# Optimization experiments

Hardware: AMD Instinct MI355X
Metric: run time of the kernel (lower is better)

## Reference

```python
import jax, jax.numpy as jnp
import numpy as np

N, E, H = 50000, 800000, 128
EIN = 2 * H + 1  # edge MLP input: h[row] | h[col] | radial_norm


def _mk(key, shape, scale=0.02):
    return jax.random.normal(key, shape, dtype=jnp.float32) * scale


def setup_inputs() -> dict:
    key = jax.random.key(0)
    ks = jax.random.split(key, 20)
    h = jax.random.normal(ks[0], (N, H), dtype=jnp.float32)
    pos = jax.random.normal(ks[1], (N, 3), dtype=jnp.float32)
    edge_index = jax.random.randint(ks[2], (2, E), 0, N, dtype=jnp.int64)
    return {
        "h": h, "pos": pos, "edge_index": edge_index,
        # edge_mlp: Linear(EIN,H) -> SiLU -> Linear(H,H)
        "We1": _mk(ks[3], (H, EIN)), "be1": jnp.zeros((H,), jnp.float32),
        "We2": _mk(ks[4], (H, H)),   "be2": jnp.zeros((H,), jnp.float32),
        # node_mlp: Linear(2H,H) -> SiLU -> Linear(H,H)
        "Wn1": _mk(ks[5], (H, 2 * H)), "bn1": jnp.zeros((H,), jnp.float32),
        "Wn2": _mk(ks[6], (H, H)),     "bn2": jnp.zeros((H,), jnp.float32),
        # coord_mlp: Linear(H,H) -> SiLU -> Linear(H,1)
        "Wc1": _mk(ks[7], (H, H)), "bc1": jnp.zeros((H,), jnp.float32),
        "Wc2": _mk(ks[8], (1, H)), "bc2": jnp.zeros((1,), jnp.float32),
    }


def reference(h, pos, edge_index, We1, be1, We2, be2, Wn1, bn1, Wn2, bn2, Wc1, bc1, Wc2, bc2):
    row, col = edge_index[0], edge_index[1]
    radial = pos[row] - pos[col]                                   # [E,3]
    radial_norm = jnp.maximum(
        jnp.linalg.norm(radial, axis=-1, keepdims=True), 1e-8)     # [E,1]
    edge_input = jnp.concatenate([h[row], h[col], radial_norm], -1)  # [E,2H+1]
    m_ij = jax.nn.silu(edge_input @ We1.T + be1) @ We2.T + be2      # [E,H]
    agg = jax.ops.segment_sum(m_ij, row, num_segments=h.shape[0])   # [N,H]
    node_in = jnp.concatenate([h, agg], -1)                         # [N,2H]
    h_new = h + (jax.nn.silu(node_in @ Wn1.T + bn1) @ Wn2.T + bn2)
    coord_diff = jnp.tanh(jax.nn.silu(m_ij @ Wc1.T + bc1) @ Wc2.T + bc2) * 0.1  # [E,1]
    coord_update = coord_diff * (radial / radial_norm)              # [E,3]
    pos_new = pos.at[row].add(coord_update)
    return h_new, pos_new
```

## Files before the change

### kernel.cpp

```cpp
#include <hip/hip_runtime.h>
#include <math.h>

#define N_NODES 50000
#define N_EDGES 800000
#define H 128
#define EIN 257
#define EPB 64
#define NWG_EDGE (N_EDGES / EPB)
#define CNT_PAD 50176
#define NBS 196

typedef short bf16x8 __attribute__((ext_vector_type(8)));
typedef short bf16x4 __attribute__((ext_vector_type(4)));
typedef short bf16x2 __attribute__((ext_vector_type(2)));
typedef float f32x4 __attribute__((ext_vector_type(4)));

static __device__ __forceinline__ short f2bf(float x) {
    unsigned u = __builtin_bit_cast(unsigned, x);
    unsigned r = (u + 0x7FFFu + ((u >> 16) & 1u)) >> 16;
    return (short)r;
}

static __device__ __forceinline__ short f2bfr(float x) {
    return (short)((__builtin_bit_cast(unsigned, x) + 0x8000u) >> 16);
}

static __device__ __forceinline__ float bf2f(short s) {
    return __builtin_bit_cast(float, ((unsigned)(unsigned short)s) << 16);
}

static __device__ __forceinline__ float silu(float x) {
#if __has_builtin(__builtin_amdgcn_rcpf)
    return x * __builtin_amdgcn_rcpf(1.0f + __expf(-x));
#else
    return x / (1.0f + __expf(-x));
#endif
}

static __device__ __forceinline__ void pk_agg_add(unsigned* addr, unsigned val) {
#if __has_builtin(__builtin_amdgcn_global_atomic_fadd_v2bf16)
    bf16x2 v = __builtin_bit_cast(bf16x2, val);
    (void)__builtin_amdgcn_global_atomic_fadd_v2bf16(
        (__attribute__((address_space(1))) bf16x2*)(unsigned long long)addr, v);
#else
    asm volatile("global_atomic_pk_add_bf16 %0, %1, off"
                 :: "v"(addr), "v"(val) : "memory");
#endif
}

#define P_W1  (128*264)
#define P_W2  (128*128)
#define P_TOT (2*(P_W1 + P_W2))
#define NH4   (N_NODES * H / 4)
#define AGG16 (N_NODES * H * 2 / 16)
#define POS4  ((N_NODES * 3 + 3) / 4)
#define NW3   (128*128)
#define PROJ_NB ((N_NODES + 63) / 64)

__global__ __launch_bounds__(256) void prep_w(
    const float* __restrict__ We1, const float* __restrict__ We2,
    const float* __restrict__ Wc1, const float* __restrict__ be2,
    const float* __restrict__ bc1,
    const float* __restrict__ Wn1, const float* __restrict__ Wn2,
    short* __restrict__ W1b, short* __restrict__ W2b, short* __restrict__ W3b,
    short* __restrict__ Wn1b, short* __restrict__ Wn2b,
    float* __restrict__ w256f, float* __restrict__ bc1p,
    unsigned* __restrict__ cnt, int cntn)
{
    int i = blockIdx.x * 256 + threadIdx.x;
    if (i < P_TOT) {
        if (i < P_W1) {
            int j = i / 264, k = i % 264;
            W1b[i] = (k < EIN) ? f2bf(We1[j * EIN + k]) : (short)0;
        } else if (i < P_W1 + P_W2) {
            int t = i - P_W1;
            W2b[t] = f2bf(We2[t]);
        } else if (i < 2 * P_W1 + P_W2) {
            int t = i - P_W1 - P_W2;
            int j = t / 264, k = t % 264;
            Wn1b[t] = (k < 256) ? f2bf(Wn1[j * 256 + k]) : (short)0;
        } else {
            int t = i - 2 * P_W1 - P_W2;
            Wn2b[t] = f2bf(Wn2[t]);
        }
        return;
    }
    i -= P_TOT;
    if (i < 128) { w256f[i] = We1[i * EIN + 256]; return; }
    i -= 128;
    if (i < NW3) {
        int j = i >> 7, k = i & 127;
        const float* wr = &Wc1[j * 128];
        float acc = 0.f;
        #pragma unroll 8
        for (int o = 0; o < 128; ++o)
            acc += wr[o] * We2[o * 128 + k];
        W3b[i] = f2bf(acc);
        return;
    }
    i -= NW3;
    if (i < 128) {
        const float* wr = &Wc1[i * 128];
        float acc = bc1[i];
        #pragma unroll 8
        for (int o = 0; o < 128; ++o) acc += wr[o] * be2[o];
        bc1p[i] = acc;
        return;
    }
    i -= 128;
    if (cnt && i < cntn) cnt[i] = 0u;
}

template<bool PROJ_ON>
__global__ __launch_bounds__(256) void prep2(
    int proj_nb,
    const float* __restrict__ h, const short* __restrict__ W1b,
    const float* __restrict__ be1,
    short* __restrict__ Abf, short* __restrict__ Bbf,
    int nh4, short* __restrict__ hbf,
    uint4* __restrict__ aggz, int aggz_n,
    float4* __restrict__ pos_dst, const float4* __restrict__ pos_src,
    const int* __restrict__ erow, unsigned* __restrict__ cnt)
{
    const int tid = threadIdx.x;
    if (PROJ_ON && (int)blockIdx.x < proj_nb) {
        __shared__ short hh[64][136];
        const int nb = blockIdx.x * 64;
        {
            const int rlane = tid & 15;
            const int row0  = tid >> 4;
            #pragma unroll
            for (int it = 0; it < 4; ++it) {
                int rr = row0 + it * 16;
                int node = nb + rr;
                if (node >= N_NODES) node = N_NODES - 1;
                const float4* src = (const float4*)&h[(size_t)node * H + rlane * 8];
                float4 a = src[0], b = src[1];
                bf16x8 v = { f2bf(a.x), f2bf(a.y), f2bf(a.z), f2bf(a.w),
                             f2bf(b.x), f2bf(b.y), f2bf(b.z), f2bf(b.w) };
                *(bf16x8*)&hh[rr][rlane * 8] = v;
            }
        }
        __syncthreads();

        const int lane = tid & 63;
        const int q    = lane >> 4;
        const int l15  = lane & 15;
        const int n0   = (tid >> 6) * 32;

        f32x4 accA[2][4] = {}, accB[2][4] = {};
        #pragma unroll
        for (int ks = 0; ks < 4; ++ks) {
            int k0 = ks * 32 + q * 8;
            bf16x8 wa0 = *(const bf16x8*)&W1b[(n0 + l15) * 264 + k0];
            bf16x8 wa1 = *(const bf16x8*)&W1b[(n0 + 16 + l15) * 264 + k0];
            bf16x8 wb0 = *(const bf16x8*)&W1b[(n0 + l15) * 264 + 128 + k0];
            bf16x8 wb1 = *(const bf16x8*)&W1b[(n0 + 16 + l15) * 264 + 128 + k0];
            bf16x8 e0 = *(const bf16x8*)&hh[l15][k0];
            bf16x8 e1 = *(const bf16x8*)&hh[16 + l15][k0];
// ... 64 lines not shown
    unsigned v = (i < N_NODES) ? cnt[i] : 0u;
    unsigned orig = v;
    #pragma unroll
    for (int d = 1; d < 64; d <<= 1) {
        unsigned n = __shfl_up(v, d);
        if ((t & 63) >= d) v += n;
    }
    __shared__ unsigned wsum[4], woff[4];
    if ((t & 63) == 63) wsum[t >> 6] = v;
    __syncthreads();
    if (t == 0) {
        unsigned r = 0;
        #pragma unroll
        for (int k = 0; k < 4; ++k) { woff[k] = r; r += wsum[k]; }
    }
    __syncthreads();
    unsigned incl = v + woff[t >> 6];
    offs[i] = incl - orig;
    if (t == 255) bsum[blockIdx.x] = incl;
}

__global__ __launch_bounds__(256) void scatter_edges(const int* __restrict__ eidx,
        unsigned* __restrict__ offs, const unsigned* __restrict__ bsum,
        int2* __restrict__ es) {
    __shared__ unsigned sb[256];
    __shared__ unsigned wsum[4], woff[4];
    int t = threadIdx.x;
    unsigned v = (t < NBS) ? bsum[t] : 0u;
    unsigned orig = v;
    #pragma unroll
    for (int d = 1; d < 64; d <<= 1) {
        unsigned n = __shfl_up(v, d);
        if ((t & 63) >= d) v += n;
    }
    if ((t & 63) == 63) wsum[t >> 6] = v;
    __syncthreads();
    if (t == 0) {
        unsigned r = 0;
        #pragma unroll
        for (int k = 0; k < 4; ++k) { woff[k] = r; r += wsum[k]; }
    }
    __syncthreads();
    sb[t] = v + woff[t >> 6] - orig;
    __syncthreads();
    int e = blockIdx.x * 256 + t;
    if (e < N_EDGES) {
        int r = eidx[e];
        unsigned p = atomicAdd(&offs[r], 1u) + sb[r >> 8];
        es[p] = int2{r, eidx[N_EDGES + e]};
    }
}

template<bool AGGBF16, bool SORTED, bool PROJ>
__global__ __launch_bounds__(256, 4) void edge_kernel(
    const short* __restrict__ hbf,
    const short* __restrict__ Abf, const short* __restrict__ Bbf,
    const float* __restrict__ pos,
    const int2* __restrict__ es,
    const int* __restrict__ rsrc, const int* __restrict__ csrc,
    const float* __restrict__ w256f, const float* __restrict__ be1,
    const float* __restrict__ be2, const float* __restrict__ bc1p,
    const float* __restrict__ wc2f, const float* __restrict__ bc2,
    const short* __restrict__ W1b, const short* __restrict__ W2b,
    const short* __restrict__ W3b,
    unsigned* __restrict__ aggb,
    float* __restrict__ aggf,
    float* __restrict__ pos_out)
{
    __shared__ union {
        short ein[EPB][264];
        struct { short t[EPB][136]; short m[EPB][136]; } p;
    } s_u;
    __shared__ float s_rn[EPB];
    __shared__ float s_unit[EPB][3];
    __shared__ int   s_row[EPB];
    __shared__ int   s_col[EPB];
    __shared__ float s_dot[EPB];

    const int tid = threadIdx.x;

    int wg;
    {
        const int Q = NWG_EDGE >> 3, R = NWG_EDGE & 7;
        int x = blockIdx.x & 7, k = blockIdx.x >> 3;
        int start = (x < R) ? x * (Q + 1) : R * (Q + 1) + (x - R) * Q;
        wg = start + k;
    }
    const int eb = wg * EPB;

    if (tid < EPB) {
        int ge = eb + tid;
        int r, c;
        if constexpr (SORTED) { int2 rc = es[ge]; r = rc.x; c = rc.y; }
        else { r = rsrc[ge]; c = csrc[ge]; }
        s_row[tid] = r;
        s_col[tid] = c;
        float dx = pos[r*3+0] - pos[c*3+0];
        float dy = pos[r*3+1] - pos[c*3+1];
        float dz = pos[r*3+2] - pos[c*3+2];
        float nrm = sqrtf(dx*dx + dy*dy + dz*dz);
        float rn  = fmaxf(nrm, 1e-8f);
        s_rn[tid] = rn;
        s_unit[tid][0] = dx / rn;
        s_unit[tid][1] = dy / rn;
        s_unit[tid][2] = dz / rn;
        s_dot[tid] = 0.0f;
    }
    __syncthreads();

    const int lane = tid & 63;
    const int q    = lane >> 4;
    const int l15  = lane & 15;
    const int n0   = (tid >> 6) * 32;
    const int w    = tid >> 6;
    const int rlane = tid & 15;
    const int row0  = tid >> 4;

    if constexpr (PROJ) {
        float4 wv0 = *(const float4*)&w256f[rlane * 8];
        float4 wv1 = *(const float4*)&w256f[rlane * 8 + 4];
        float wv[8] = { wv0.x, wv0.y, wv0.z, wv0.w, wv1.x, wv1.y, wv1.z, wv1.w };
        #pragma unroll
        for (int it = 0; it < 4; ++it) {
            int e = row0 + it * 16;
            bf16x8 a = *(const bf16x8*)&Abf[(size_t)s_row[e] * H + rlane * 8];
            bf16x8 b = *(const bf16x8*)&Bbf[(size_t)s_col[e] * H + rlane * 8];
            float rn = s_rn[e];
            bf16x8 t8;
            #pragma unroll
            for (int j = 0; j < 8; ++j) {
                float x = bf2f(a[j]) + bf2f(b[j]) + rn * wv[j];
                t8[j] = f2bfr(silu(x));
            }
            *(bf16x8*)&s_u.p.t[e][rlane * 8] = t8;
        }
    } else {
        #pragma unroll
        for (int it = 0; it < 8; ++it) {
            int rr = row0 + it * 16;
            int e  = rr & 63, sg = rr >> 6;
            int idx = sg ? s_col[e] : s_row[e];
            bf16x8 v = *(const bf16x8*)&hbf[(size_t)idx * H + rlane * 8];
            *(bf16x8*)&s_u.ein[e][sg * 128 + rlane * 8] = v;
        }
        __syncthreads();

        f32x4 acc[2][4] = {};
        #pragma unroll
        for (int ks = 0; ks < 8; ++ks) {
            int k0 = ks * 32 + q * 8;
            bf16x8 w0 = *(const bf16x8*)&W1b[(n0 + l15) * 264 + k0];
            bf16x8 w1 = *(const bf16x8*)&W1b[(n0 + 16 + l15) * 264 + k0];
            bf16x8 e0 = *(const bf16x8*)&s_u.ein[l15][k0];
            bf16x8 e1 = *(const bf16x8*)&s_u.ein[16 + l15][k0];
            bf16x8 e2 = *(const bf16x8*)&s_u.ein[32 + l15][k0];
            bf16x8 e3 = *(const bf16x8*)&s_u.ein[48 + l15][k0];
            acc[0][0] = __builtin_amdgcn_mfma_f32_16x16x32_bf16(w0, e0, acc[0][0], 0, 0, 0);
            acc[0][1] = __builtin_amdgcn_mfma_f32_16x16x32_bf16(w0, e1, acc[0][1], 0, 0, 0);
            acc[0][2] = __builtin_amdgcn_mfma_f32_16x16x32_bf16(w0, e2, acc[0][2], 0, 0, 0);
            acc[0][3] = __builtin_amdgcn_mfma_f32_16x16x32_bf16(w0, e3, acc[0][3], 0, 0, 0);
            acc[1][0] = __builtin_amdgcn_mfma_f32_16x16x32_bf16(w1, e0, acc[1][0], 0, 0, 0);
            acc[1][1] = __builtin_amdgcn_mfma_f32_16x16x32_bf16(w1, e1, acc[1][1], 0, 0, 0);
            acc[1][2] = __builtin_amdgcn_mfma_f32_16x16x32_bf16(w1, e2, acc[1][2], 0, 0, 0);
            acc[1][3] = __builtin_amdgcn_mfma_f32_16x16x32_bf16(w1, e3, acc[1][3], 0, 0, 0);
        }
        float w256v[2][4], b1v[2][4], rn_e[4];
        #pragma unroll
        for (int ct = 0; ct < 2; ++ct)
            #pragma unroll
            for (int r = 0; r < 4; ++r) {
                int ch = n0 + ct * 16 + q * 4 + r;
                w256v[ct][r] = w256f[ch];
                b1v[ct][r]   = be1[ch];
            }
        #pragma unroll
        for (int et = 0; et < 4; ++et) rn_e[et] = s_rn[et * 16 + l15];

        bf16x4 tv[2][4];
        #pragma unroll
        for (int ct = 0; ct < 2; ++ct)
            #pragma unroll
            for (int et = 0; et < 4; ++et) {
                bf16x4 v;
                #pragma unroll
                for (int r = 0; r < 4; ++r)
                    v[r] = f2bfr(silu(acc[ct][et][r] + rn_e[et] * w256v[ct][r] + b1v[ct][r]));
                tv[ct][et] = v;
            }
        __syncthreads();
        #pragma unroll
        for (int ct = 0; ct < 2; ++ct)
            #pragma unroll
            for (int et = 0; et < 4; ++et)
                *(bf16x4*)&s_u.p.t[et * 16 + l15][n0 + ct * 16 + q * 4] = tv[ct][et];
    }
    __syncthreads();

    f32x4 acc2[2][4] = {}, acc3[2][4] = {};
    #pragma unroll
    for (int ks = 0; ks < 4; ++ks) {
        int k0 = ks * 32 + q * 8;
        bf16x8 w20 = *(const bf16x8*)&W2b[(n0 + l15) * 128 + k0];
        bf16x8 w21 = *(const bf16x8*)&W2b[(n0 + 16 + l15) * 128 + k0];
        bf16x8 w30 = *(const bf16x8*)&W3b[(n0 + l15) * 128 + k0];
        bf16x8 w31 = *(const bf16x8*)&W3b[(n0 + 16 + l15) * 128 + k0];
        bf16x8 e0 = *(const bf16x8*)&s_u.p.t[l15][k0];
        bf16x8 e1 = *(const bf16x8*)&s_u.p.t[16 + l15][k0];
        bf16x8 e2 = *(const bf16x8*)&s_u.p.t[32 + l15][k0];
        bf16x8 e3 = *(const bf16x8*)&s_u.p.t[48 + l15][k0];
        acc2[0][0] = __builtin_amdgcn_mfma_f32_16x16x32_bf16(w20, e0, acc2[0][0], 0, 0, 0);
        acc2[0][1] = __builtin_amdgcn_mfma_f32_16x16x32_bf16(w20, e1, acc2[0][1], 0, 0, 0);
        acc2[0][2] = __builtin_amdgcn_mfma_f32_16x16x32_bf16(w20, e2, acc2[0][2], 0, 0, 0);
        acc2[0][3] = __builtin_amdgcn_mfma_f32_16x16x32_bf16(w20, e3, acc2[0][3], 0, 0, 0);
        acc2[1][0] = __builtin_amdgcn_mfma_f32_16x16x32_bf16(w21, e0, acc2[1][0], 0, 0, 0);
        acc2[1][1] = __builtin_amdgcn_mfma_f32_16x16x32_bf16(w21, e1, acc2[1][1], 0, 0, 0);
        acc2[1][2] = __builtin_amdgcn_mfma_f32_16x16x32_bf16(w21, e2, acc2[1][2], 0, 0, 0);
        acc2[1][3] = __builtin_amdgcn_mfma_f32_16x16x32_bf16(w21, e3, acc2[1][3], 0, 0, 0);
        acc3[0][0] = __builtin_amdgcn_mfma_f32_16x16x32_bf16(w30, e0, acc3[0][0], 0, 0, 0);
        acc3[0][1] = __builtin_amdgcn_mfma_f32_16x16x32_bf16(w30, e1, acc3[0][1], 0, 0, 0);
        acc3[0][2] = __builtin_amdgcn_mfma_f32_16x16x32_bf16(w30, e2, acc3[0][2], 0, 0, 0);
        acc3[0][3] = __builtin_amdgcn_mfma_f32_16x16x32_bf16(w30, e3, acc3[0][3], 0, 0, 0);
        acc3[1][0] = __builtin_amdgcn_mfma_f32_16x16x32_bf16(w31, e0, acc3[1][0], 0, 0, 0);
        acc3[1][1] = __builtin_amdgcn_mfma_f32_16x16x32_bf16(w31, e1, acc3[1][1], 0, 0, 0);
        acc3[1][2] = __builtin_amdgcn_mfma_f32_16x16x32_bf16(w31, e2, acc3[1][2], 0, 0, 0);
        acc3[1][3] = __builtin_amdgcn_mfma_f32_16x16x32_bf16(w31, e3, acc3[1][3], 0, 0, 0);
    }

    {
        float b2v[2][4];
        #pragma unroll
        for (int ct = 0; ct < 2; ++ct)
            #pragma unroll
            for (int r = 0; r < 4; ++r)
                b2v[ct][r] = be2[n0 + ct * 16 + q * 4 + r];
        #pragma unroll
        for (int ct = 0; ct < 2; ++ct)
            #pragma unroll
            for (int et = 0; et < 4; ++et) {
                bf16x4 v;
                #pragma unroll
                for (int r = 0; r < 4; ++r)
                    v[r] = f2bfr(acc2[ct][et][r] + b2v[ct][r]);
                *(bf16x4*)&s_u.p.m[et * 16 + l15][n0 + ct * 16 + q * 4] = v;
            }
    }

    {
        float p[4] = {0.f, 0.f, 0.f, 0.f};
        #pragma unroll
        for (int ct = 0; ct < 2; ++ct)
            #pragma unroll
            for (int r = 0; r < 4; ++r) {
                int ch = n0 + ct * 16 + q * 4 + r;
                float bias = bc1p[ch];
                float w2   = wc2f[ch];
                #pragma unroll
                for (int et = 0; et < 4; ++et)
                    p[et] += silu(acc3[ct][et][r] + bias) * w2;
            }
        #pragma unroll
        for (int et = 0; et < 4; ++et) {
            float v = p[et];
            v += __shfl_xor(v, 16);
            v += __shfl_xor(v, 32);
            if (q == et) atomicAdd(&s_dot[et * 16 + l15], v);
        }
    }
    __syncthreads();

    if constexpr (AGGBF16) {
        const int base = w * 16;
        float a0 = 0.f, a1 = 0.f;
        int cur = s_row[base];
        #pragma unroll
        for (int i = 0; i < 16; ++i) {
            int nd = s_row[base + i];
            if (nd != cur) {
                unsigned pk = ((unsigned)(unsigned short)f2bfr(a0)) |
                              (((unsigned)(unsigned short)f2bfr(a1)) << 16);
                pk_agg_add(&aggb[(size_t)cur * 64 + lane], pk);
                a0 = 0.f; a1 = 0.f; cur = nd;
            }
            unsigned pr = *(const unsigned*)&s_u.p.m[base + i][lane * 2];
            a0 += __builtin_bit_cast(float, pr << 16);
            a1 += __builtin_bit_cast(float, pr & 0xFFFF0000u);
        }
        unsigned pk = ((unsigned)(unsigned short)f2bfr(a0)) |
                      (((unsigned)(unsigned short)f2bfr(a1)) << 16);
        pk_agg_add(&aggb[(size_t)cur * 64 + lane], pk);
    } else {
        #pragma unroll
        for (int i = 0; i < 16; ++i) {
            int row = w + i * 4;
            unsigned pr = *(const unsigned*)&s_u.p.m[row][lane * 2];
            float f0 = __builtin_bit_cast(float, pr << 16);
            float f1 = __builtin_bit_cast(float, pr & 0xFFFF0000u);
            float* dst = &aggf[(size_t)s_row[row] * H + 2 * lane];
            atomicAdd(dst, f0);
            atomicAdd(dst + 1, f1);
        }
    }

    if (tid < EPB) {
        float s = tanhf(s_dot[tid] + bc2[0]) * 0.1f;
        s_unit[tid][0] *= s;
        s_unit[tid][1] *= s;
        s_unit[tid][2] *= s;
    }
    __syncthreads();
    if (tid < EPB) {
        int r = s_row[tid];
        bool last = (tid == EPB - 1) || (s_row[tid + 1] != r);
        if (last) {
            float sx = 0.f, sy = 0.f, sz = 0.f;
            for (int j = tid; j >= 0 && s_row[j] == r; --j) {
                sx += s_unit[j][0];
                sy += s_unit[j][1];
                sz += s_unit[j][2];
            }
            atomicAdd(&pos_out[r * 3 + 0], sx);
            atomicAdd(&pos_out[r * 3 + 1], sy);
            atomicAdd(&pos_out[r * 3 + 2], sz);
        }
    }
}

template<bool AGGBF16>
__global__ __launch_bounds__(256) void node_kernel(
    const float* __restrict__ h,
    const unsigned short* __restrict__ aggb, const float* __restrict__ aggf,
    const float* __restrict__ bn1, const float* __restrict__ bn2,
    const short* __restrict__ Wn1b, const short* __restrict__ Wn2b,
    float* __restrict__ hout)
{
    __shared__ short s_a[64][264];
    __shared__ short s_t[64][136];

    const int tid = threadIdx.x;
    const int nb  = blockIdx.x * 64;

    {
        const int rlane = tid & 15;
        const int row0  = tid >> 4;
        #pragma unroll
        for (int it = 0; it < 8; ++it) {
            int rr = row0 + it * 16;
            int e  = rr & 63, sg = rr >> 6;
            int node = nb + e;
            if (node >= N_NODES) node = N_NODES - 1;
            bf16x8 v;
            if (sg == 0) {
                const float4* src = (const float4*)&h[(size_t)node * H + rlane * 8];
                float4 a = src[0], b = src[1];
                v = bf16x8{ f2bf(a.x), f2bf(a.y), f2bf(a.z), f2bf(a.w),
                            f2bf(b.x), f2bf(b.y), f2bf(b.z), f2bf(b.w) };
            } else if constexpr (AGGBF16) {
                v = *(const bf16x8*)&aggb[(size_t)node * H + rlane * 8];
            } else {
                const float* src = &aggf[(size_t)node * H + rlane * 8];
                bf16x8 t;
                #pragma unroll
                for (int j = 0; j < 8; ++j) t[j] = f2bfr(src[j]);
                v = t;
            }
            *(bf16x8*)&s_a[e][sg * 128 + rlane * 8] = v;
        }
    }
    __syncthreads();

    const int lane = tid & 63;
    const int q    = lane >> 4;
    const int l15  = lane & 15;
    const int n0   = (tid >> 6) * 32;

    f32x4 acc[2][4] = {};
    #pragma unroll
    for (int ks = 0; ks < 8; ++ks) {
        int k0 = ks * 32 + q * 8;
        bf16x8 w0 = *(const bf16x8*)&Wn1b[(n0 + l15) * 264 + k0];
        bf16x8 w1 = *(const bf16x8*)&Wn1b[(n0 + 16 + l15) * 264 + k0];
        bf16x8 e0 = *(const bf16x8*)&s_a[l15][k0];
        bf16x8 e1 = *(const bf16x8*)&s_a[16 + l15][k0];
        bf16x8 e2 = *(const bf16x8*)&s_a[32 + l15][k0];
        bf16x8 e3 = *(const bf16x8*)&s_a[48 + l15][k0];
        acc[0][0] = __builtin_amdgcn_mfma_f32_16x16x32_bf16(w0, e0, acc[0][0], 0, 0, 0);
        acc[0][1] = __builtin_amdgcn_mfma_f32_16x16x32_bf16(w0, e1, acc[0][1], 0, 0, 0);
        acc[0][2] = __builtin_amdgcn_mfma_f32_16x16x32_bf16(w0, e2, acc[0][2], 0, 0, 0);
        acc[0][3] = __builtin_amdgcn_mfma_f32_16x16x32_bf16(w0, e3, acc[0][3], 0, 0, 0);
        acc[1][0] = __builtin_amdgcn_mfma_f32_16x16x32_bf16(w1, e0, acc[1][0], 0, 0, 0);
        acc[1][1] = __builtin_amdgcn_mfma_f32_16x16x32_bf16(w1, e1, acc[1][1], 0, 0, 0);
        acc[1][2] = __builtin_amdgcn_mfma_f32_16x16x32_bf16(w1, e2, acc[1][2], 0, 0, 0);
        acc[1][3] = __builtin_amdgcn_mfma_f32_16x16x32_bf16(w1, e3, acc[1][3], 0, 0, 0);
    }
    {
        float b1v[2][4];
        #pragma unroll
        for (int ct = 0; ct < 2; ++ct)
            #pragma unroll
            for (int r = 0; r < 4; ++r)
                b1v[ct][r] = bn1[n0 + ct * 16 + q * 4 + r];
        #pragma unroll
        for (int ct = 0; ct < 2; ++ct)
            #pragma unroll
            for (int et = 0; et < 4; ++et) {
                bf16x4 v;
                #pragma unroll
                for (int r = 0; r < 4; ++r)
                    v[r] = f2bfr(silu(acc[ct][et][r] + b1v[ct][r]));
                *(bf16x4*)&s_t[et * 16 + l15][n0 + ct * 16 + q * 4] = v;
            }
    }
    __syncthreads();

    f32x4 acc2[2][4] = {};
    #pragma unroll
    for (int ks = 0; ks < 4; ++ks) {
        int k0 = ks * 32 + q * 8;
        bf16x8 w0 = *(const bf16x8*)&Wn2b[(n0 + l15) * 128 + k0];
        bf16x8 w1 = *(const bf16x8*)&Wn2b[(n0 + 16 + l15) * 128 + k0];
        bf16x8 e0 = *(const bf16x8*)&s_t[l15][k0];
        bf16x8 e1 = *(const bf16x8*)&s_t[16 + l15][k0];
        bf16x8 e2 = *(const bf16x8*)&s_t[32 + l15][k0];
        bf16x8 e3 = *(const bf16x8*)&s_t[48 + l15][k0];
        acc2[0][0] = __builtin_amdgcn_mfma_f32_16x16x32_bf16(w0, e0, acc2[0][0], 0, 0, 0);
        acc2[0][1] = __builtin_amdgcn_mfma_f32_16x16x32_bf16(w0, e1, acc2[0][1], 0, 0, 0);
        acc2[0][2] = __builtin_amdgcn_mfma_f32_16x16x32_bf16(w0, e2, acc2[0][2], 0, 0, 0);
        acc2[0][3] = __builtin_amdgcn_mfma_f32_16x16x32_bf16(w0, e3, acc2[0][3], 0, 0, 0);
        acc2[1][0] = __builtin_amdgcn_mfma_f32_16x16x32_bf16(w1, e0, acc2[1][0], 0, 0, 0);
        acc2[1][1] = __builtin_amdgcn_mfma_f32_16x16x32_bf16(w1, e1, acc2[1][1], 0, 0, 0);
        acc2[1][2] = __builtin_amdgcn_mfma_f32_16x16x32_bf16(w1, e2, acc2[1][2], 0, 0, 0);
        acc2[1][3] = __builtin_amdgcn_mfma_f32_16x16x32_bf16(w1, e3, acc2[1][3], 0, 0, 0);
    }
    {
        float b2v[2][4];
        #pragma unroll
        for (int ct = 0; ct < 2; ++ct)
            #pragma unroll
            for (int r = 0; r < 4; ++r)
                b2v[ct][r] = bn2[n0 + ct * 16 + q * 4 + r];
        #pragma unroll
        for (int ct = 0; ct < 2; ++ct)
            #pragma unroll
            for (int et = 0; et < 4; ++et) {
                int node = nb + et * 16 + l15;
                if (node < N_NODES) {
                    int ch0 = n0 + ct * 16 + q * 4;
                    const float4 hres = *(const float4*)&h[(size_t)node * H + ch0];
                    float4 o;
                    o.x = acc2[ct][et][0] + b2v[ct][0] + hres.x;
                    o.y = acc2[ct][et][1] + b2v[ct][1] + hres.y;
                    o.z = acc2[ct][et][2] + b2v[ct][2] + hres.z;
                    o.w = acc2[ct][et][3] + b2v[ct][3] + hres.w;
                    *(float4*)&hout[(size_t)node * H + ch0] = o;
                }
            }
    }
}

extern "C" void kernel_launch(void* const* d_in, const int* in_sizes, int n_in,
                              void* d_out, int out_size, void* d_ws, size_t ws_size,
                              hipStream_t stream) {
    const float* h   = (const float*)d_in[0];
    const float* pos = (const float*)d_in[1];
    const int*  eidx = (const int*)d_in[2];
    const float* We1 = (const float*)d_in[3];
    const float* be1 = (const float*)d_in[4];
    const float* We2 = (const float*)d_in[5];
    const float* be2 = (const float*)d_in[6];
    const float* Wn1 = (const float*)d_in[7];
    const float* bn1 = (const float*)d_in[8];
    const float* Wn2 = (const float*)d_in[9];
    const float* bn2 = (const float*)d_in[10];
    const float* Wc1 = (const float*)d_in[11];
    const float* bc1 = (const float*)d_in[12];
    const float* Wc2 = (const float*)d_in[13];
    const float* bc2 = (const float*)d_in[14];

    float* out_h   = (float*)d_out;
    float* out_pos = out_h + (size_t)N_NODES * H;

    char* ws = (char*)d_ws;
    short* W1b  = (short*)(ws);
    short* W2b  = (short*)(ws + 2 * P_W1);
    short* W3b  = (short*)(ws + 2 * (P_W1 + P_W2));
    short* Wn1b = (short*)(ws + 2 * (P_W1 + 2 * P_W2));
    short* Wn2b = (short*)(ws + 2 * (2 * P_W1 + 2 * P_W2));
    float* w256f = (float*)(ws + 2 * (size_t)(2 * P_W1 + 3 * P_W2));
    float* bc1p  = w256f + 128;
    const size_t WSW = 2 * (size_t)(2 * P_W1 + 3 * P_W2) + 1024;
    const size_t HBF = (size_t)N_NODES * H * 2;
    const size_t AGG = (size_t)N_NODES * H * 2;
    const size_t CNTB = (size_t)CNT_PAD * 4;
    const size_t BSB  = 256 * 4;
    const size_t ESB  = (size_t)N_EDGES * 8;
    const size_t PRJ  = (size_t)N_NODES * H * 2;
    short* hbf = (short*)(ws + WSW);
    const bool use_bf16 = (ws_size >= WSW + HBF + AGG);
    const bool use_sort = (ws_size >= WSW + HBF + AGG + CNTB + BSB + ESB);
    const bool use_proj = (ws_size >= WSW + HBF + AGG + CNTB + BSB + ESB + 2 * PRJ);

    const int PW_N  = P_TOT + 128 + NW3 + 128;

    if (use_bf16) {
        unsigned* aggb = (unsigned*)(ws + WSW + HBF);
        if (use_sort) {
            unsigned* cnt  = (unsigned*)(ws + WSW + HBF + AGG);
            unsigned* bsum = (unsigned*)((char*)cnt + CNTB);
            int2* es = (int2*)((char*)bsum + BSB);
            short* Abf = (short*)((char*)es + ESB);
            short* Bbf = (short*)((char*)Abf + PRJ);

            prep_w<<<(PW_N + CNT_PAD + 255) / 256, 256, 0, stream>>>(
                We1, We2, Wc1, be2, bc1, Wn1, Wn2,
                W1b, W2b, W3b, Wn1b, Wn2b, w256f, bc1p, cnt, CNT_PAD);
            if (use_proj) {
                const int rest = AGG16 + POS4 + N_EDGES;
                prep2<true><<<PROJ_NB + (rest + 255) / 256, 256, 0, stream>>>(
                    PROJ_NB, h, W1b, be1, Abf, Bbf, 0, nullptr,
                    (uint4*)aggb, AGG16, (float4*)out_pos, (const float4*)pos,
                    eidx, cnt);
            } else {
                const int rest = NH4 + AGG16 + POS4 + N_EDGES;
                prep2<false><<<(rest + 255) / 256, 256, 0, stream>>>(
                    0, h, nullptr, nullptr, nullptr, nullptr, NH4, hbf,
                    (uint4*)aggb, AGG16, (float4*)out_pos, (const float4*)pos,
                    eidx, cnt);
            }
            scan1<<<NBS, 256, 0, stream>>>(cnt, cnt, bsum);
            scatter_edges<<<(N_EDGES + 255) / 256, 256, 0, stream>>>(eidx, cnt, bsum, es);
            if (use_proj)
                edge_kernel<true, true, true><<<NWG_EDGE, 256, 0, stream>>>(
                    hbf, Abf, Bbf, pos, es, nullptr, nullptr,
                    w256f, be1, be2, bc1p, Wc2, bc2,
                    W1b, W2b, W3b, aggb, nullptr, out_pos);
            else
                edge_kernel<true, true, false><<<NWG_EDGE, 256, 0, stream>>>(
                    hbf, nullptr, nullptr, pos, es, nullptr, nullptr,
                    w256f, be1, be2, bc1p, Wc2, bc2,
                    W1b, W2b, W3b, aggb, nullptr, out_pos);
        } else {
            prep_w<<<(PW_N + 255) / 256, 256, 0, stream>>>(
                We1, We2, Wc1, be2, bc1, Wn1, Wn2,
                W1b, W2b, W3b, Wn1b, Wn2b, w256f, bc1p, nullptr, 0);
            const int rest = NH4 + AGG16 + POS4;
            prep2<false><<<(rest + 255) / 256, 256, 0, stream>>>(
                0, h, nullptr, nullptr, nullptr, nullptr, NH4, hbf,
                (uint4*)aggb, AGG16, (float4*)out_pos, (const float4*)pos,
                nullptr, nullptr);
            edge_kernel<true, false, false><<<NWG_EDGE, 256, 0, stream>>>(
                hbf, nullptr, nullptr, pos, nullptr, eidx, eidx + N_EDGES,
                w256f, be1, be2, bc1p, Wc2, bc2,
                W1b, W2b, W3b, aggb, nullptr, out_pos);
        }
        node_kernel<true><<<(N_NODES + 63) / 64, 256, 0, stream>>>(
            h, (const unsigned short*)aggb, nullptr,
            bn1, bn2, Wn1b, Wn2b, out_h);
    } else {
        prep_w<<<(PW_N + 255) / 256, 256, 0, stream>>>(
            We1, We2, Wc1, be2, bc1, Wn1, Wn2,
            W1b, W2b, W3b, Wn1b, Wn2b, w256f, bc1p, nullptr, 0);
        const int rest = NH4 + POS4;
        prep2<false><<<(rest + 255) / 256, 256, 0, stream>>>(
            0, h, nullptr, nullptr, nullptr, nullptr, NH4, hbf,
            nullptr, 0, (float4*)out_pos, (const float4*)pos,
            nullptr, nullptr);
        hipMemsetAsync(out_h, 0, (size_t)N_NODES * H * sizeof(float), stream);
        edge_kernel<false, false, false><<<NWG_EDGE, 256, 0, stream>>>(
            hbf, nullptr, nullptr, pos, nullptr, eidx, eidx + N_EDGES,
            w256f, be1, be2, bc1p, Wc2, bc2,
            W1b, W2b, W3b, nullptr, out_h, out_pos);
        node_kernel<false><<<(N_NODES + 63) / 64, 256, 0, stream>>>(
            h, nullptr, out_h, bn1, bn2, Wn1b, Wn2b, out_h);
    }
}
```

Baseline: 412.7 us.

## Fold second edge-MLP layer into node MLP, aggregate pre-activation edge hidden state

Linearity lets segment_sum be pushed through We2: the edge kernel now scatters the silu hidden state t instead of m_ij. The node kernel uses Wn1·We2 as a folded weight and adds degree × (Wn1·be2) as a bias. This removes the per-edge W2 GEMM and the m staging in LDS on the projection path, keeping only the coord GEMM. A separate offsets buffer keeps the raw degree counts, and launch bounds rise to 8 waves per SIMD because LDS use drops. The fold adds bf16 rounding in a different place, and the higher occupancy target may force register spills.

New measurement: 354.3 us. 14.1% less time.

```diff
diff --git a/kernel.cpp b/kernel.cpp
--- a/kernel.cpp
+++ b/kernel.cpp
@@ -65,7 +65,8 @@
     short* __restrict__ W1b, short* __restrict__ W2b, short* __restrict__ W3b,
     short* __restrict__ Wn1b, short* __restrict__ Wn2b,
     float* __restrict__ w256f, float* __restrict__ bc1p,
-    unsigned* __restrict__ cnt, int cntn)
+    float* __restrict__ bfold,
+    unsigned* __restrict__ cnt, int cntn, int fold)
 {
     int i = blockIdx.x * 256 + threadIdx.x;
     if (i < P_TOT) {
@@ -78,7 +79,19 @@
         } else if (i < 2 * P_W1 + P_W2) {
             int t = i - P_W1 - P_W2;
             int j = t / 264, k = t % 264;
-            Wn1b[t] = (k < 256) ? f2bf(Wn1[j * 256 + k]) : (short)0;
+            short v;
+            if (k < 128) v = f2bf(Wn1[j * 256 + k]);
+            else if (k < 256) {
+                if (fold) {
+                    const float* wr = &Wn1[j * 256 + 128];
+                    const float* wc = &We2[k - 128];
+                    float acc = 0.f;
+                    #pragma unroll 8
+                    for (int o = 0; o < 128; ++o) acc += wr[o] * wc[o * 128];
+                    v = f2bf(acc);
+                } else v = f2bf(Wn1[j * 256 + k]);
+            } else v = 0;
+            Wn1b[t] = v;
         } else {
             int t = i - 2 * P_W1 - P_W2;
             Wn2b[t] = f2bf(Wn2[t]);
@@ -105,6 +118,15 @@
         #pragma unroll 8
         for (int o = 0; o < 128; ++o) acc += wr[o] * be2[o];
         bc1p[i] = acc;
+        return;
+    }
+    i -= 128;
+    if (i < 128) {
+        const float* wr = &Wn1[i * 256 + 128];
+        float acc = 0.f;
+        #pragma unroll 8
+        for (int o = 0; o < 128; ++o) acc += wr[o] * be2[o];
+        bfold[i] = acc;
         return;
     }
     i -= 128;
@@ -275,7 +297,7 @@
 }
 
 template<bool AGGBF16, bool SORTED, bool PROJ>
-__global__ __launch_bounds__(256, 4) void edge_kernel(
+__global__ __launch_bounds__(256, 8) void edge_kernel(
     const short* __restrict__ hbf,
     const short* __restrict__ Abf, const short* __restrict__ Bbf,
     const float* __restrict__ pos,
@@ -290,10 +312,7 @@
     float* __restrict__ aggf,
     float* __restrict__ pos_out)
 {
-    __shared__ union {
-        short ein[EPB][264];
-        struct { short t[EPB][136]; short m[EPB][136]; } p;
-    } s_u;
+    __shared__ short s_t[EPB][136];
     __shared__ float s_rn[EPB];
     __shared__ float s_unit[EPB][3];
     __shared__ int   s_row[EPB];
@@ -355,16 +374,83 @@
                 float x = bf2f(a[j]) + bf2f(b[j]) + rn * wv[j];
                 t8[j] = f2bfr(silu(x));
             }
-            *(bf16x8*)&s_u.p.t[e][rlane * 8] = t8;
-        }
+            *(bf16x8*)&s_t[e][rlane * 8] = t8;
+        }
+        __syncthreads();
+
+        {
+            const int base = w * 16;
+            float a0 = 0.f, a1 = 0.f;
+            int cur = s_row[base];
+            #pragma unroll
+            for (int i = 0; i < 16; ++i) {
+                int nd = s_row[base + i];
+                if (nd != cur) {
+                    unsigned pk = ((unsigned)(unsigned short)f2bfr(a0)) |
+                                  (((unsigned)(unsigned short)f2bfr(a1)) << 16);
+                    pk_agg_add(&aggb[(size_t)cur * 64 + lane], pk);
+                    a0 = 0.f; a1 = 0.f; cur = nd;
+                }
+                unsigned pr = *(const unsigned*)&s_t[base + i][lane * 2];
+                a0 += __builtin_bit_cast(float, pr << 16);
+                a1 += __builtin_bit_cast(float, pr & 0xFFFF0000u);
+            }
+            unsigned pk = ((unsigned)(unsigned short)f2bfr(a0)) |
+                          (((unsigned)(unsigned short)f2bfr(a1)) << 16);
+            pk_agg_add(&aggb[(size_t)cur * 64 + lane], pk);
+        }
+
+        f32x4 acc3[2][4] = {};
+        #pragma unroll
+        for (int ks = 0; ks < 4; ++ks) {
+            int k0 = ks * 32 + q * 8;
+            bf16x8 w30 = *(const bf16x8*)&W3b[(n0 + l15) * 128 + k0];
+            bf16x8 w31 = *(const bf16x8*)&W3b[(n0 + 16 + l15) * 128 + k0];
+            bf16x8 e0 = *(const bf16x8*)&s_t[l15][k0];
+            bf16x8 e1 = *(const bf16x8*)&s_t[16 + l15][k0];
+            bf16x8 e2 = *(const bf16x8*)&s_t[32 + l15][k0];
+            bf16x8 e3 = *(const bf16x8*)&s_t[48 + l15][k0];
+            acc3[0][0] = __builtin_amdgcn_mfma_f32_16x16x32_bf16(w30, e0, acc3[0][0], 0, 0, 0);
+            acc3[0][1] = __builtin_amdgcn_mfma_f32_16x16x32_bf16(w30, e1, acc3[0][1], 0, 0, 0);
+            acc3[0][2] = __builtin_amdgcn_mfma_f32_16x16x32_bf16(w30, e2, acc3[0][2], 0, 0, 0);
+            acc3[0][3] = __builtin_amdgcn_mfma_f32_16x16x32_bf16(w30, e3, acc3[0][3], 0, 0, 0);
+            acc3[1][0] = __builtin_amdgcn_mfma_f32_16x16x32_bf16(w31, e0, acc3[1][0], 0, 0, 0);
+            acc3[1][1] = __builtin_amdgcn_mfma_f32_16x16x32_bf16(w31, e1, acc3[1][1], 0, 0, 0);
+            acc3[1][2] = __builtin_amdgcn_mfma_f32_16x16x32_bf16(w31, e2, acc3[1][2], 0, 0, 0);
+            acc3[1][3] = __builtin_amdgcn_mfma_f32_16x16x32_bf16(w31, e3, acc3[1][3], 0, 0, 0);
+        }
+        {
+            float p[4] = {0.f, 0.f, 0.f, 0.f};
+            #pragma unroll
+            for (int ct = 0; ct < 2; ++ct)
+                #pragma unroll
+                for (int r = 0; r < 4; ++r) {
+                    int ch = n0 + ct * 16 + q * 4 + r;
+                    float bias = bc1p[ch];
+                    float w2   = wc2f[ch];
+                    #pragma unroll
+                    for (int et = 0; et < 4; ++et)
+                        p[et] += silu(acc3[ct][et][r] + bias) * w2;
+                }
+            #pragma unroll
+            for (int et = 0; et < 4; ++et) {
+                float v = p[et];
+                v += __shfl_xor(v, 16);
+                v += __shfl_xor(v, 32);
+                if (q == et) atomicAdd(&s_dot[et * 16 + l15], v);
+            }
+        }
+        __syncthreads();
     } else {
+        __shared__ short s_ein[EPB][264];
+        __shared__ short s_m[EPB][136];
         #pragma unroll
         for (int it = 0; it < 8; ++it) {
             int rr = row0 + it * 16;
             int e  = rr & 63, sg = rr >> 6;
             int idx = sg ? s_col[e] : s_row[e];
             bf16x8 v = *(const bf16x8*)&hbf[(size_t)idx * H + rlane * 8];
-            *(bf16x8*)&s_u.ein[e][sg * 128 + rlane * 8] = v;
+            *(bf16x8*)&s_ein[e][sg * 128 + rlane * 8] = v;
         }
         __syncthreads();
 
@@ -374,10 +460,10 @@
             int k0 = ks * 32 + q * 8;
             bf16x8 w0 = *(const bf16x8*)&W1b[(n0 + l15) * 264 + k0];
             bf16x8 w1 = *(const bf16x8*)&W1b[(n0 + 16 + l15) * 264 + k0];
-            bf16x8 e0 = *(const bf16x8*)&s_u.ein[l15][k0];
-            bf16x8 e1 = *(const bf16x8*)&s_u.ein[16 + l15][k0];
-            bf16x8 e2 = *(const bf16x8*)&s_u.ein[32 + l15][k0];
-            bf16x8 e3 = *(const bf16x8*)&s_u.ein[48 + l15][k0];
+            bf16x8 e0 = *(const bf16x8*)&s_ein[l15][k0];
+            bf16x8 e1 = *(const bf16x8*)&s_ein[16 + l15][k0];
+            bf16x8 e2 = *(const bf16x8*)&s_ein[32 + l15][k0];
+            bf16x8 e3 = *(const bf16x8*)&s_ein[48 + l15][k0];
             acc[0][0] = __builtin_amdgcn_mfma_f32_16x16x32_bf16(w0, e0, acc[0][0], 0, 0, 0);
             acc[0][1] = __builtin_amdgcn_mfma_f32_16x16x32_bf16(w0, e1, acc[0][1], 0, 0, 0);
             acc[0][2] = __builtin_amdgcn_mfma_f32_16x16x32_bf16(w0, e2, acc[0][2], 0, 0, 0);
@@ -387,140 +473,132 @@
             acc[1][2] = __builtin_amdgcn_mfma_f32_16x16x32_bf16(w1, e2, acc[1][2], 0, 0, 0);
             acc[1][3] = __builtin_amdgcn_mfma_f32_16x16x32_bf16(w1, e3, acc[1][3], 0, 0, 0);
         }
-        float w256v[2][4], b1v[2][4], rn_e[4];
-        #pragma unroll
-        for (int ct = 0; ct < 2; ++ct)
-            #pragma unroll
-            for (int r = 0; r < 4; ++r) {
-                int ch = n0 + ct * 16 + q * 4 + r;
-                w256v[ct][r] = w256f[ch];
-                b1v[ct][r]   = be1[ch];
-            }
-        #pragma unroll
-        for (int et = 0; et < 4; ++et) rn_e[et] = s_rn[et * 16 + l15];
-
-        bf16x4 tv[2][4];
-        #pragma unroll
-        for (int ct = 0; ct < 2; ++ct)
-            #pragma unroll
-            for (int et = 0; et < 4; ++et) {
-                bf16x4 v;
+        {
+            float w256v[2][4], b1v[2][4], rn_e[4];
+            #pragma unroll
+            for (int ct = 0; ct < 2; ++ct)
+                #pragma unroll
+                for (int r = 0; r < 4; ++r) {
+                    int ch = n0 + ct * 16 + q * 4 + r;
+                    w256v[ct][r] = w256f[ch];
+                    b1v[ct][r]   = be1[ch];
+                }
+            #pragma unroll
+            for (int et = 0; et < 4; ++et) rn_e[et] = s_rn[et * 16 + l15];
+            #pragma unroll
+            for (int ct = 0; ct < 2; ++ct)
+                #pragma unroll
+                for (int et = 0; et < 4; ++et) {
+                    bf16x4 v;
+                    #pragma unroll
+                    for (int r = 0; r < 4; ++r)
+                        v[r] = f2bfr(silu(acc[ct][et][r] + rn_e[et] * w256v[ct][r] + b1v[ct][r]));
+                    *(bf16x4*)&s_t[et * 16 + l15][n0 + ct * 16 + q * 4] = v;
+                }
+        }
+        __syncthreads();
+
+        f32x4 acc2[2][4] = {}, acc3[2][4] = {};
+        #pragma unroll
+        for (int ks = 0; ks < 4; ++ks) {
+            int k0 = ks * 32 + q * 8;
+            bf16x8 w20 = *(const bf16x8*)&W2b[(n0 + l15) * 128 + k0];
+            bf16x8 w21 = *(const bf16x8*)&W2b[(n0 + 16 + l15) * 128 + k0];
+            bf16x8 w30 = *(const bf16x8*)&W3b[(n0 + l15) * 128 + k0];
+            bf16x8 w31 = *(const bf16x8*)&W3b[(n0 + 16 + l15) * 128 + k0];
+            bf16x8 e0 = *(const bf16x8*)&s_t[l15][k0];
+            bf16x8 e1 = *(const bf16x8*)&s_t[16 + l15][k0];
+            bf16x8 e2 = *(const bf16x8*)&s_t[32 + l15][k0];
+            bf16x8 e3 = *(const bf16x8*)&s_t[48 + l15][k0];
+            acc2[0][0] = __builtin_amdgcn_mfma_f32_16x16x32_bf16(w20, e0, acc2[0][0], 0, 0, 0);
+            acc2[0][1] = __builtin_amdgcn_mfma_f32_16x16x32_bf16(w20, e1, acc2[0][1], 0, 0, 0);
+            acc2[0][2] = __builtin_amdgcn_mfma_f32_16x16x32_bf16(w20, e2, acc2[0][2], 0, 0, 0);
+            acc2[0][3] = __builtin_amdgcn_mfma_f32_16x16x32_bf16(w20, e3, acc2[0][3], 0, 0, 0);
+            acc2[1][0] = __builtin_amdgcn_mfma_f32_16x16x32_bf16(w21, e0, acc2[1][0], 0, 0, 0);
+            acc2[1][1] = __builtin_amdgcn_mfma_f32_16x16x32_bf16(w21, e1, acc2[1][1], 0, 0, 0);
+            acc2[1][2] = __builtin_amdgcn_mfma_f32_16x16x32_bf16(w21, e2, acc2[1][2], 0, 0, 0);
+            acc2[1][3] = __builtin_amdgcn_mfma_f32_16x16x32_bf16(w21, e3, acc2[1][3], 0, 0, 0);
+            acc3[0][0] = __builtin_amdgcn_mfma_f32_16x16x32_bf16(w30, e0, acc3[0][0], 0, 0, 0);
+            acc3[0][1] = __builtin_amdgcn_mfma_f32_16x16x32_bf16(w30, e1, acc3[0][1], 0, 0, 0);
+            acc3[0][2] = __builtin_amdgcn_mfma_f32_16x16x32_bf16(w30, e2, acc3[0][2], 0, 0, 0);
+            acc3[0][3] = __builtin_amdgcn_mfma_f32_16x16x32_bf16(w30, e3, acc3[0][3], 0, 0, 0);
+            acc3[1][0] = __builtin_amdgcn_mfma_f32_16x16x32_bf16(w31, e0, acc3[1][0], 0, 0, 0);
+            acc3[1][1] = __builtin_amdgcn_mfma_f32_16x16x32_bf16(w31, e1, acc3[1][1], 0, 0, 0);
+            acc3[1][2] = __builtin_amdgcn_mfma_f32_16x16x32_bf16(w31, e2, acc3[1][2], 0, 0, 0);
+            acc3[1][3] = __builtin_amdgcn_mfma_f32_16x16x32_bf16(w31, e3, acc3[1][3], 0, 0, 0);
+        }
+        {
+            float b2v[2][4];
+            #pragma unroll
+            for (int ct = 0; ct < 2; ++ct)
                 #pragma unroll
                 for (int r = 0; r < 4; ++r)
-                    v[r] = f2bfr(silu(acc[ct][et][r] + rn_e[et] * w256v[ct][r] + b1v[ct][r]));
-                tv[ct][et] = v;
-            }
+                    b2v[ct][r] = be2[n0 + ct * 16 + q * 4 + r];
+            #pragma unroll
+            for (int ct = 0; ct < 2; ++ct)
+                #pragma unroll
+                for (int et = 0; et < 4; ++et) {
+                    bf16x4 v;
+                    #pragma unroll
+                    for (int r = 0; r < 4; ++r)
+                        v[r] = f2bfr(acc2[ct][et][r] + b2v[ct][r]);
+                    *(bf16x4*)&s_m[et * 16 + l15][n0 + ct * 16 + q * 4] = v;
+                }
+        }
+        {
+            float p[4] = {0.f, 0.f, 0.f, 0.f};
+            #pragma unroll
+            for (int ct = 0; ct < 2; ++ct)
+                #pragma unroll
+                for (int r = 0; r < 4; ++r) {
+                    int ch = n0 + ct * 16 + q * 4 + r;
+                    float bias = bc1p[ch];
+                    float w2   = wc2f[ch];
+                    #pragma unroll
+                    for (int et = 0; et < 4; ++et)
+                        p[et] += silu(acc3[ct][et][r] + bias) * w2;
+                }
+            #pragma unroll
+            for (int et = 0; et < 4; ++et) {
+                float v = p[et];
+                v += __shfl_xor(v, 16);
+                v += __shfl_xor(v, 32);
+                if (q == et) atomicAdd(&s_dot[et * 16 + l15], v);
+            }
+        }
         __syncthreads();
-        #pragma unroll
-        for (int ct = 0; ct < 2; ++ct)
-            #pragma unroll
-            for (int et = 0; et < 4; ++et)
-                *(bf16x4*)&s_u.p.t[et * 16 + l15][n0 + ct * 16 + q * 4] = tv[ct][et];
-    }
-    __syncthreads();
-
-    f32x4 acc2[2][4] = {}, acc3[2][4] = {};
-    #pragma unroll
-    for (int ks = 0; ks < 4; ++ks) {
-        int k0 = ks * 32 + q * 8;
-        bf16x8 w20 = *(const bf16x8*)&W2b[(n0 + l15) * 128 + k0];
-        bf16x8 w21 = *(const bf16x8*)&W2b[(n0 + 16 + l15) * 128 + k0];
-        bf16x8 w30 = *(const bf16x8*)&W3b[(n0 + l15) * 128 + k0];
-        bf16x8 w31 = *(const bf16x8*)&W3b[(n0 + 16 + l15) * 128 + k0];
-        bf16x8 e0 = *(const bf16x8*)&s_u.p.t[l15][k0];
-        bf16x8 e1 = *(const bf16x8*)&s_u.p.t[16 + l15][k0];
-        bf16x8 e2 = *(const bf16x8*)&s_u.p.t[32 + l15][k0];
-        bf16x8 e3 = *(const bf16x8*)&s_u.p.t[48 + l15][k0];
-        acc2[0][0] = __builtin_amdgcn_mfma_f32_16x16x32_bf16(w20, e0, acc2[0][0], 0, 0, 0);
-        acc2[0][1] = __builtin_amdgcn_mfma_f32_16x16x32_bf16(w20, e1, acc2[0][1], 0, 0, 0);
-        acc2[0][2] = __builtin_amdgcn_mfma_f32_16x16x32_bf16(w20, e2, acc2[0][2], 0, 0, 0);
-        acc2[0][3] = __builtin_amdgcn_mfma_f32_16x16x32_bf16(w20, e3, acc2[0][3], 0, 0, 0);
-        acc2[1][0] = __builtin_amdgcn_mfma_f32_16x16x32_bf16(w21, e0, acc2[1][0], 0, 0, 0);
-        acc2[1][1] = __builtin_amdgcn_mfma_f32_16x16x32_bf16(w21, e1, acc2[1][1], 0, 0, 0);
-        acc2[1][2] = __builtin_amdgcn_mfma_f32_16x16x32_bf16(w21, e2, acc2[1][2], 0, 0, 0);
-        acc2[1][3] = __builtin_amdgcn_mfma_f32_16x16x32_bf16(w21, e3, acc2[1][3], 0, 0, 0);
-        acc3[0][0] = __builtin_amdgcn_mfma_f32_16x16x32_bf16(w30, e0, acc3[0][0], 0, 0, 0);
-        acc3[0][1] = __builtin_amdgcn_mfma_f32_16x16x32_bf16(w30, e1, acc3[0][1], 0, 0, 0);
-        acc3[0][2] = __builtin_amdgcn_mfma_f32_16x16x32_bf16(w30, e2, acc3[0][2], 0, 0, 0);
-        acc3[0][3] = __builtin_amdgcn_mfma_f32_16x16x32_bf16(w30, e3, acc3[0][3], 0, 0, 0);
-        acc3[1][0] = __builtin_amdgcn_mfma_f32_16x16x32_bf16(w31, e0, acc3[1][0], 0, 0, 0);
-        acc3[1][1] = __builtin_amdgcn_mfma_f32_16x16x32_bf16(w31, e1, acc3[1][1], 0, 0, 0);
-        acc3[1][2] = __builtin_amdgcn_mfma_f32_16x16x32_bf16(w31, e2, acc3[1][2], 0, 0, 0);
-        acc3[1][3] = __builtin_amdgcn_mfma_f32_16x16x32_bf16(w31, e3, acc3[1][3], 0, 0, 0);
-    }
-
-    {
-        float b2v[2][4];
-        #pragma unroll
-        for (int ct = 0; ct < 2; ++ct)
-            #pragma unroll
-            for (int r = 0; r < 4; ++r)
-                b2v[ct][r] = be2[n0 + ct * 16 + q * 4 + r];
-        #pragma unroll
-        for (int ct = 0; ct < 2; ++ct)
-            #pragma unroll
-            for (int et = 0; et < 4; ++et) {
-                bf16x4 v;
-                #pragma unroll
-                for (int r = 0; r < 4; ++r)
-                    v[r] = f2bfr(acc2[ct][et][r] + b2v[ct][r]);
-                *(bf16x4*)&s_u.p.m[et * 16 + l15][n0 + ct * 16 + q * 4] = v;
-            }
-    }
-
-    {
-        float p[4] = {0.f, 0.f, 0.f, 0.f};
-        #pragma unroll
-        for (int ct = 0; ct < 2; ++ct)
-            #pragma unroll
-            for (int r = 0; r < 4; ++r) {
-                int ch = n0 + ct * 16 + q * 4 + r;
-                float bias = bc1p[ch];
-                float w2   = wc2f[ch];
-                #pragma unroll
-                for (int et = 0; et < 4; ++et)
-                    p[et] += silu(acc3[ct][et][r] + bias) * w2;
-            }
-        #pragma unroll
-        for (int et = 0; et < 4; ++et) {
-            float v = p[et];
-            v += __shfl_xor(v, 16);
-            v += __shfl_xor(v, 32);
-            if (q == et) atomicAdd(&s_dot[et * 16 + l15], v);
-        }
-    }
-    __syncthreads();
-
-    if constexpr (AGGBF16) {
-        const int base = w * 16;
-        float a0 = 0.f, a1 = 0.f;
-        int cur = s_row[base];
-        #pragma unroll
-        for (int i = 0; i < 16; ++i) {
-            int nd = s_row[base + i];
-            if (nd != cur) {
-                unsigned pk = ((unsigned)(unsigned short)f2bfr(a0)) |
-                              (((unsigned)(unsigned short)f2bfr(a1)) << 16);
-                pk_agg_add(&aggb[(size_t)cur * 64 + lane], pk);
-                a0 = 0.f; a1 = 0.f; cur = nd;
-            }
-            unsigned pr = *(const unsigned*)&s_u.p.m[base + i][lane * 2];
-            a0 += __builtin_bit_cast(float, pr << 16);
-            a1 += __builtin_bit_cast(float, pr & 0xFFFF0000u);
-        }
-        unsigned pk = ((unsigned)(unsigned short)f2bfr(a0)) |
-                      (((unsigned)(unsigned short)f2bfr(a1)) << 16);
-        pk_agg_add(&aggb[(size_t)cur * 64 + lane], pk);
-    } else {
-        #pragma unroll
-        for (int i = 0; i < 16; ++i) {
-            int row = w + i * 4;
-            unsigned pr = *(const unsigned*)&s_u.p.m[row][lane * 2];
-            float f0 = __builtin_bit_cast(float, pr << 16);
-            float f1 = __builtin_bit_cast(float, pr & 0xFFFF0000u);
-            float* dst = &aggf[(size_t)s_row[row] * H + 2 * lane];
-            atomicAdd(dst, f0);
-            atomicAdd(dst + 1, f1);
+
+        if constexpr (AGGBF16) {
+            const int base = w * 16;
+            float a0 = 0.f, a1 = 0.f;
+            int cur = s_row[base];
+            #pragma unroll
+            for (int i = 0; i < 16; ++i) {
+                int nd = s_row[base + i];
+                if (nd != cur) {
+                    unsigned pk = ((unsigned)(unsigned short)f2bfr(a0)) |
+                                  (((unsigned)(unsigned short)f2bfr(a1)) << 16);
+                    pk_agg_add(&aggb[(size_t)cur * 64 + lane], pk);
+                    a0 = 0.f; a1 = 0.f; cur = nd;
+                }
+                unsigned pr = *(const unsigned*)&s_m[base + i][lane * 2];
+                a0 += __builtin_bit_cast(float, pr << 16);
+                a1 += __builtin_bit_cast(float, pr & 0xFFFF0000u);
+            }
+            unsigned pk = ((unsigned)(unsigned short)f2bfr(a0)) |
+                          (((unsigned)(unsigned short)f2bfr(a1)) << 16);
+            pk_agg_add(&aggb[(size_t)cur * 64 + lane], pk);
+        } else {
+            #pragma unroll
+            for (int i = 0; i < 16; ++i) {
+                int row = w + i * 4;
+                unsigned pr = *(const unsigned*)&s_m[row][lane * 2];
+                float f0 = __builtin_bit_cast(float, pr << 16);
+                float f1 = __builtin_bit_cast(float, pr & 0xFFFF0000u);
+                float* dst = &aggf[(size_t)s_row[row] * H + 2 * lane];
+                atomicAdd(dst, f0);
+                atomicAdd(dst + 1, f1);
+            }
         }
     }
 
@@ -548,10 +626,11 @@
     }
 }
 
-template<bool AGGBF16>
+template<bool AGGBF16, bool FOLD>
 __global__ __launch_bounds__(256) void node_kernel(
     const float* __restrict__ h,
     const unsigned short* __restrict__ aggb, const float* __restrict__ aggf,
+    const unsigned* __restrict__ deg, const float* __restrict__ bfold,
     const float* __restrict__ bn1, const float* __restrict__ bn2,
     const short* __restrict__ Wn1b, const short* __restrict__ Wn2b,
     float* __restrict__ hout)
@@ -616,20 +695,34 @@
         acc[1][3] = __builtin_amdgcn_mfma_f32_16x16x32_bf16(w1, e3, acc[1][3], 0, 0, 0);
     }
     {
-        float b1v[2][4];
+        float b1v[2][4], bf_v[2][4], degf[4];
         #pragma unroll
         for (int ct = 0; ct < 2; ++ct)
             #pragma unroll
-            for (int r = 0; r < 4; ++r)
-                b1v[ct][r] = bn1[n0 + ct * 16 + q * 4 + r];
+            for (int r = 0; r < 4; ++r) {
+                int ch = n0 + ct * 16 + q * 4 + r;
+                b1v[ct][r] = bn1[ch];
+                if constexpr (FOLD) bf_v[ct][r] = bfold[ch];
+            }
+        if constexpr (FOLD) {
+            #pragma unroll
+            for (int et = 0; et < 4; ++et) {
+                int node = nb + et * 16 + l15;
+                if (node >= N_NODES) node = N_NODES - 1;
+                degf[et] = (float)deg[node];
+            }
+        }
         #pragma unroll
         for (int ct = 0; ct < 2; ++ct)
             #pragma unroll
             for (int et = 0; et < 4; ++et) {
                 bf16x4 v;
                 #pragma unroll
-                for (int r = 0; r < 4; ++r)
-                    v[r] = f2bfr(silu(acc[ct][et][r] + b1v[ct][r]));
+                for (int r = 0; r < 4; ++r) {
+                    float x = acc[ct][et][r] + b1v[ct][r];
+                    if constexpr (FOLD) x += degf[et] * bf_v[ct][r];
+                    v[r] = f2bfr(silu(x));
+                }
                 *(bf16x4*)&s_t[et * 16 + l15][n0 + ct * 16 + q * 4] = v;
             }
     }
@@ -710,32 +803,36 @@
     short* Wn2b = (short*)(ws + 2 * (2 * P_W1 + 2 * P_W2));
     float* w256f = (float*)(ws + 2 * (size_t)(2 * P_W1 + 3 * P_W2));
     float* bc1p  = w256f + 128;
-    const size_t WSW = 2 * (size_t)(2 * P_W1 + 3 * P_W2) + 1024;
+    float* bfold = w256f + 256;
+    const size_t WSW = 2 * (size_t)(2 * P_W1 + 3 * P_W2) + 2048;
     const size_t HBF = (size_t)N_NODES * H * 2;
     const size_t AGG = (size_t)N_NODES * H * 2;
     const size_t CNTB = (size_t)CNT_PAD * 4;
+    const size_t OFFB = (size_t)CNT_PAD * 4;
     const size_t BSB  = 256 * 4;
     const size_t ESB  = (size_t)N_EDGES * 8;
     const size_t PRJ  = (size_t)N_NODES * H * 2;
     short* hbf = (short*)(ws + WSW);
     const bool use_bf16 = (ws_size >= WSW + HBF + AGG);
-    const bool use_sort = (ws_size >= WSW + HBF + AGG + CNTB + BSB + ESB);
-    const bool use_proj = (ws_size >= WSW + HBF + AGG + CNTB + BSB + ESB + 2 * PRJ);
-
-    const int PW_N  = P_TOT + 128 + NW3 + 128;
+    const bool use_sort = (ws_size >= WSW + HBF + AGG + CNTB + OFFB + BSB + ESB);
+    const bool use_proj = (ws_size >= WSW + HBF + AGG + CNTB + OFFB + BSB + ESB + 2 * PRJ);
+
+    const int PW_N = P_TOT + 128 + NW3 + 128 + 128;
 
     if (use_bf16) {
         unsigned* aggb = (unsigned*)(ws + WSW + HBF);
         if (use_sort) {
             unsigned* cnt  = (unsigned*)(ws + WSW + HBF + AGG);
-            unsigned* bsum = (unsigned*)((char*)cnt + CNTB);
+            unsigned* offs = (unsigned*)((char*)cnt + CNTB);
+            unsigned* bsum = (unsigned*)((char*)offs + OFFB);
             int2* es = (int2*)((char*)bsum + BSB);
             short* Abf = (short*)((char*)es + ESB);
             short* Bbf = (short*)((char*)Abf + PRJ);
 
             prep_w<<<(PW_N + CNT_PAD + 255) / 256, 256, 0, stream>>>(
                 We1, We2, Wc1, be2, bc1, Wn1, Wn2,
-                W1b, W2b, W3b, Wn1b, Wn2b, w256f, bc1p, cnt, CNT_PAD);
+                W1b, W2b, W3b, Wn1b, Wn2b, w256f, bc1p, bfold,
+                cnt, CNT_PAD, use_proj ? 1 : 0);
             if (use_proj) {
                 const int rest = AGG16 + POS4 + N_EDGES;
                 prep2<true><<<PROJ_NB + (rest + 255) / 256, 256, 0, stream>>>(
@@ -749,22 +846,30 @@
                     (uint4*)aggb, AGG16, (float4*)out_pos, (const float4*)pos,
                     eidx, cnt);
             }
-            scan1<<<NBS, 256, 0, stream>>>(cnt, cnt, bsum);
-            scatter_edges<<<(N_EDGES + 255) / 256, 256, 0, stream>>>(eidx, cnt, bsum, es);
-            if (use_proj)
+            scan1<<<NBS, 256, 0, stream>>>(cnt, offs, bsum);
+            scatter_edges<<<(N_EDGES + 255) / 256, 256, 0, stream>>>(eidx, offs, bsum, es);
+            if (use_proj) {
                 edge_kernel<true, true, true><<<NWG_EDGE, 256, 0, stream>>>(
                     hbf, Abf, Bbf, pos, es, nullptr, nullptr,
                     w256f, be1, be2, bc1p, Wc2, bc2,
                     W1b, W2b, W3b, aggb, nullptr, out_pos);
-            else
+                node_kernel<true, true><<<(N_NODES + 63) / 64, 256, 0, stream>>>(
+                    h, (const unsigned short*)aggb, nullptr, cnt, bfold,
+                    bn1, bn2, Wn1b, Wn2b, out_h);
+            } else {
                 edge_kernel<true, true, false><<<NWG_EDGE, 256, 0, stream>>>(
                     hbf, nullptr, nullptr, pos, es, nullptr, nullptr,
                     w256f, be1, be2, bc1p, Wc2, bc2,
                     W1b, W2b, W3b, aggb, nullptr, out_pos);
+                node_kernel<true, false><<<(N_NODES + 63) / 64, 256, 0, stream>>>(
+                    h, (const unsigned short*)aggb, nullptr, nullptr, nullptr,
+                    bn1, bn2, Wn1b, Wn2b, out_h);
+            }
         } else {
             prep_w<<<(PW_N + 255) / 256, 256, 0, stream>>>(
                 We1, We2, Wc1, be2, bc1, Wn1, Wn2,
-                W1b, W2b, W3b, Wn1b, Wn2b, w256f, bc1p, nullptr, 0);
+                W1b, W2b, W3b, Wn1b, Wn2b, w256f, bc1p, bfold,
+                nullptr, 0, 0);
             const int rest = NH4 + AGG16 + POS4;
             prep2<false><<<(rest + 255) / 256, 256, 0, stream>>>(
                 0, h, nullptr, nullptr, nullptr, nullptr, NH4, hbf,
@@ -774,14 +879,15 @@
                 hbf, nullptr, nullptr, pos, nullptr, eidx, eidx + N_EDGES,
                 w256f, be1, be2, bc1p, Wc2, bc2,
                 W1b, W2b, W3b, aggb, nullptr, out_pos);
-        }
-        node_kernel<true><<<(N_NODES + 63) / 64, 256, 0, stream>>>(
-            h, (const unsigned short*)aggb, nullptr,
-            bn1, bn2, Wn1b, Wn2b, out_h);
+            node_kernel<true, false><<<(N_NODES + 63) / 64, 256, 0, stream>>>(
+                h, (const unsigned short*)aggb, nullptr, nullptr, nullptr,
+                bn1, bn2, Wn1b, Wn2b, out_h);
+        }
     } else {
         prep_w<<<(PW_N + 255) / 256, 256, 0, stream>>>(
             We1, We2, Wc1, be2, bc1, Wn1, Wn2,
-            W1b, W2b, W3b, Wn1b, Wn2b, w256f, bc1p, nullptr, 0);
+            W1b, W2b, W3b, Wn1b, Wn2b, w256f, bc1p, bfold,
+            nullptr, 0, 0);
         const int rest = NH4 + POS4;
         prep2<false><<<(rest + 255) / 256, 256, 0, stream>>>(
             0, h, nullptr, nullptr, nullptr, nullptr, NH4, hbf,
@@ -792,7 +898,7 @@
             hbf, nullptr, nullptr, pos, nullptr, eidx, eidx + N_EDGES,
             w256f, be1, be2, bc1p, Wc2, bc2,
             W1b, W2b, W3b, nullptr, out_h, out_pos);
-        node_kernel<false><<<(N_NODES + 63) / 64, 256, 0, stream>>>(
-            h, nullptr, out_h, bn1, bn2, Wn1b, Wn2b, out_h);
-    }
-}
+        node_kernel<false, false><<<(N_NODES + 63) / 64, 256, 0, stream>>>(
+            h, nullptr, out_h, nullptr, nullptr, bn1, bn2, Wn1b, Wn2b, out_h);
+    }
+}
```
